# Optimization experiments

Hardware: AMD Instinct MI355X
Metric: run time of the kernel (lower is better)

## Reference

```python
import jax, jax.numpy as jnp
import numpy as np

# Qwen3.5 GatedDeltaNet config (Qwen3-Next linear-attention block)
HIDDEN = 2048
HV, HK = 32, 16          # value heads, key heads (GQA rep = 2)
DK, DV = 128, 128        # key/value head dims
KCONV = 4                # causal depthwise conv kernel
KEY_DIM = HK * DK        # 2048
VAL_DIM = HV * DV        # 4096
CONV_DIM = 2 * KEY_DIM + VAL_DIM  # 8192
EPS = 1e-6


def setup_inputs() -> dict:
    key = jax.random.key(0)
    ks = jax.random.split(key, 9)
    B, S = 2, 1024
    def w(k, shape, sc=0.02):
        return jax.random.normal(k, shape, jnp.float32) * sc
    return {
        "hidden_states": jax.random.normal(ks[0], (B, S, HIDDEN), jnp.float32),
        "conv_w": w(ks[1], (CONV_DIM, 1, KCONV), 0.1),   # depthwise conv1d weight (groups=CONV_DIM, no bias)
        "w_qkv": w(ks[2], (HIDDEN, CONV_DIM)),
        "w_z": w(ks[3], (HIDDEN, VAL_DIM)),
        "w_b": w(ks[4], (HIDDEN, HV)),
        "w_a": w(ks[5], (HIDDEN, HV)),
        "w_out": w(ks[6], (VAL_DIM, HIDDEN)),
        "dt_bias": jnp.ones((HV,), jnp.float32),
        "A_log": jnp.log(jax.random.uniform(ks[7], (HV,), jnp.float32, 1e-3, 16.0)),
        "norm_w": jnp.ones((DV,), jnp.float32),
    }


def _l2norm(x):
    return x / jnp.sqrt(jnp.sum(x * x, axis=-1, keepdims=True) + 1e-6)


def reference(hidden_states, conv_w, w_qkv, w_z, w_b, w_a, w_out, dt_bias, A_log, norm_w):
    B, S, _ = hidden_states.shape
    # input projections
    mixed = hidden_states @ w_qkv                     # [B,S,CONV_DIM]
    z = (hidden_states @ w_z).reshape(B, S, HV, DV)   # gate for RMSNormGated
    b = hidden_states @ w_b                           # [B,S,HV]
    a = hidden_states @ w_a                           # [B,S,HV]

    # causal depthwise conv1d (left pad K-1), then SiLU
    x = mixed.transpose(0, 2, 1)                      # [B,C,S]
    y = jax.lax.conv_general_dilated(
        x, conv_w, window_strides=(1,), padding=[(KCONV - 1, 0)],
        dimension_numbers=("NCH", "OIH", "NCH"), feature_group_count=CONV_DIM)
    mixed = jax.nn.silu(y).transpose(0, 2, 1)         # [B,S,CONV_DIM]

    q, k, v = jnp.split(mixed, [KEY_DIM, 2 * KEY_DIM], axis=-1)
    q = q.reshape(B, S, HK, DK)
    k = k.reshape(B, S, HK, DK)
    v = v.reshape(B, S, HV, DV)

    beta = jax.nn.sigmoid(b)                                    # [B,S,HV]
    g = -jnp.exp(A_log) * jax.nn.softplus(a + dt_bias)          # [B,S,HV], log-decay <= 0

    rep = HV // HK
    q = jnp.repeat(q, rep, axis=2)                              # [B,S,HV,DK]
    k = jnp.repeat(k, rep, axis=2)

    # use_qk_l2norm_in_kernel=True, then standard 1/sqrt(dk) scaling on q
    q = _l2norm(q) * (DK ** -0.5)
    k = _l2norm(k)

    # gated delta-rule recurrence over time (state S: [B,HV,DK,DV])
    qt = q.transpose(1, 0, 2, 3)
    kt = k.transpose(1, 0, 2, 3)
    vt = v.transpose(1, 0, 2, 3)
    gt = g.transpose(1, 0, 2)
    bt = beta.transpose(1, 0, 2)

    S0 = jnp.zeros((B, HV, DK, DV), jnp.float32)

    def step(Sm, inp):
        q_, k_, v_, g_, b_ = inp
        Sm = Sm * jnp.exp(g_)[..., None, None]                  # gated decay
        kv = jnp.einsum('bhk,bhkv->bhv', k_, Sm)                # k^T S (current memory readout)
        delta = (v_ - kv) * b_[..., None]                       # delta-rule update, scaled by beta
        Sm = Sm + jnp.einsum('bhk,bhv->bhkv', k_, delta)        # rank-1 write
        o = jnp.einsum('bhk,bhkv->bhv', q_, Sm)                 # query readout
        return Sm, o

    _, o = jax.lax.scan(step, S0, (qt, kt, vt, gt, bt))
    o = o.transpose(1, 0, 2, 3)                                 # [B,S,HV,DV]

    # RMSNormGated over head_v_dim: gate with silu(z), then RMSNorm
    og = o * jax.nn.silu(z)
    var = jnp.mean(og * og, axis=-1, keepdims=True)
    on = og * jax.lax.rsqrt(var + EPS) * norm_w

    return on.reshape(B, S, VAL_DIM) @ w_out                    # [B,S,HIDDEN]
```

## Files before the change

### kernel.cpp

```cpp
#include <hip/hip_runtime.h>
#include <hip/hip_bf16.h>
#include <cstdint>
#include <type_traits>

#define HIDDEN   2048
#define HV       32
#define HK       16
#define DK       128
#define DV       128
#define KEY_DIM  2048
#define VAL_DIM  4096
#define CONV_DIM 8192
#define NTOK     2048
#define SEQ      1024
#define N1       12288
#define C_CH     64
#define NCHK     (SEQ / C_CH)

typedef __attribute__((ext_vector_type(4))) float f4_t;
typedef __attribute__((ext_vector_type(2))) float f2_t;
typedef __attribute__((ext_vector_type(8))) short bf8_t;
typedef __attribute__((ext_vector_type(16))) float f16acc;
typedef __attribute__((ext_vector_type(4))) unsigned short u16x4;
typedef __attribute__((ext_vector_type(8))) unsigned short u16x8;
typedef __attribute__((ext_vector_type(2))) uint32_t u32x2;
typedef __attribute__((ext_vector_type(4))) uint32_t u32x4;

__device__ __forceinline__ unsigned short f2bf(float f) {
    union { float f; uint32_t u; } a; a.f = f;
    uint32_t u = a.u;
    return (unsigned short)((u + 0x7fff + ((u >> 16) & 1)) >> 16);
}
__device__ __forceinline__ float bf2f(unsigned short h) {
    uint32_t u = ((uint32_t)h) << 16;
    union { uint32_t u; float f; } a; a.u = u;
    return a.f;
}
__device__ __forceinline__ bf8_t lds_frag(const unsigned short* p) {
    u32x2 a = *(const u32x2*)p;
    u32x2 b = *(const u32x2*)(p + 4);
    u32x4 w = {a[0], a[1], b[0], b[1]};
    return __builtin_bit_cast(bf8_t, w);
}

__global__ __launch_bounds__(256) void k_cast_hs(const float* __restrict__ hs,
                                                 unsigned short* __restrict__ out) {
    int i = blockIdx.x * 256 + threadIdx.x;
    f4_t v = ((const f4_t*)hs)[i];
    u16x4 o;
    o[0] = f2bf(v[0]); o[1] = f2bf(v[1]); o[2] = f2bf(v[2]); o[3] = f2bf(v[3]);
    ((u16x4*)out)[i] = o;
}

__global__ __launch_bounds__(256) void k_trans_w1(const float* __restrict__ w_qkv,
                                                  const float* __restrict__ w_z,
                                                  unsigned short* __restrict__ w1t) {
    __shared__ float tile[32][33];
    int tx = threadIdx.x & 31, ty = threadIdx.x >> 5;
    int n0 = blockIdx.x * 32, k0 = blockIdx.y * 32;
    int n = n0 + tx;
#pragma unroll
    for (int i = 0; i < 4; i++) {
        int k = k0 + ty + i * 8;
        float v = (n < CONV_DIM) ? w_qkv[(size_t)k * CONV_DIM + n]
                                 : w_z[(size_t)k * VAL_DIM + (n - CONV_DIM)];
        tile[ty + i * 8][tx] = v;
    }
    __syncthreads();
#pragma unroll
    for (int i = 0; i < 4; i++)
        w1t[(size_t)(n0 + ty + i * 8) * HIDDEN + k0 + tx] = f2bf(tile[tx][ty + i * 8]);
}

__global__ __launch_bounds__(256) void k_trans(const float* __restrict__ src,
                                               unsigned short* __restrict__ dst,
                                               int K, int N) {
    __shared__ float tile[32][33];
    int tx = threadIdx.x & 31, ty = threadIdx.x >> 5;
    int n0 = blockIdx.x * 32, k0 = blockIdx.y * 32;
#pragma unroll
    for (int i = 0; i < 4; i++)
        tile[ty + i * 8][tx] = src[(size_t)(k0 + ty + i * 8) * N + n0 + tx];
    __syncthreads();
#pragma unroll
    for (int i = 0; i < 4; i++)
        dst[(size_t)(n0 + ty + i * 8) * K + k0 + tx] = f2bf(tile[tx][ty + i * 8]);
}

template <typename OT>
__global__ __launch_bounds__(256, 4) void k_gemm_bt(const unsigned short* __restrict__ A,
                                                    const unsigned short* __restrict__ B,
                                                    OT* __restrict__ C, int K, int N) {
    __shared__ unsigned short lA[2][128 * 32];
    __shared__ unsigned short lB[2][128 * 32];
    int tid = threadIdx.x;
    int wave = tid >> 6, lane = tid & 63;
    int nwg = gridDim.x * gridDim.y;
    int lid = blockIdx.y * gridDim.x + blockIdx.x;
    int swz = (lid & 7) * (nwg >> 3) + (lid >> 3);
    int m0 = (swz & 15) * 128, n0 = (swz >> 4) * 128;
    int wm = wave & 1, wn = wave >> 1;
    f4_t acc[4][4];
#pragma unroll
    for (int i = 0; i < 4; i++)
#pragma unroll
        for (int j = 0; j < 4; j++) acc[i][j] = (f4_t){0.f, 0.f, 0.f, 0.f};
    int srow = wave * 16 + (lane >> 2);
    int scol = ((lane & 3) ^ ((lane >> 3) & 3)) * 8;
    int quad = lane >> 4, lrow = lane & 15;
    int rswz = (lrow >> 1) & 3;

    const unsigned short* gA0 = A + (size_t)(m0 + srow) * K + scol;
    const unsigned short* gA1 = A + (size_t)(m0 + 64 + srow) * K + scol;
    const unsigned short* gB0 = B + (size_t)(n0 + srow) * K + scol;
    const unsigned short* gB1 = B + (size_t)(n0 + 64 + srow) * K + scol;

#define GEMM_STAGE(buf, k0)                                                                        \
    do {                                                                                           \
        __builtin_amdgcn_global_load_lds((const __attribute__((address_space(1))) void*)(gA0 + (k0)), \
            (__attribute__((address_space(3))) void*)(&lA[buf][wave * 512]), 16, 0, 0);            \
        __builtin_amdgcn_global_load_lds((const __attribute__((address_space(1))) void*)(gA1 + (k0)), \
            (__attribute__((address_space(3))) void*)(&lA[buf][2048 + wave * 512]), 16, 0, 0);     \
        __builtin_amdgcn_global_load_lds((const __attribute__((address_space(1))) void*)(gB0 + (k0)), \
            (__attribute__((address_space(3))) void*)(&lB[buf][wave * 512]), 16, 0, 0);            \
        __builtin_amdgcn_global_load_lds((const __attribute__((address_space(1))) void*)(gB1 + (k0)), \
            (__attribute__((address_space(3))) void*)(&lB[buf][2048 + wave * 512]), 16, 0, 0);     \
    } while (0)

    GEMM_STAGE(0, 0);
    __syncthreads();

    int cur = 0;
    for (int k0 = 0; k0 < K; k0 += 32) {
        if (k0 + 32 < K) GEMM_STAGE(cur ^ 1, k0 + 32);
        bf8_t af[4], bfv[4];
#pragma unroll
        for (int i = 0; i < 4; i++) {
            int sa = (quad ^ rswz) * 8;
            af[i]  = *(const bf8_t*)&lA[cur][(wm * 64 + i * 16 + lrow) * 32 + sa];
            bfv[i] = *(const bf8_t*)&lB[cur][(wn * 64 + i * 16 + lrow) * 32 + sa];
        }
#pragma unroll
        for (int i = 0; i < 4; i++)
#pragma unroll
            for (int j = 0; j < 4; j++)
                acc[i][j] = __builtin_amdgcn_mfma_f32_16x16x32_bf16(af[i], bfv[j], acc[i][j], 0, 0, 0);
        __syncthreads();
        cur ^= 1;
    }
#undef GEMM_STAGE
#pragma unroll
    for (int i = 0; i < 4; i++) {
        int row_b = m0 + wm * 64 + i * 16 + quad * 4;
#pragma unroll
        for (int j = 0; j < 4; j++) {
            int col = n0 + wn * 64 + j * 16 + lrow;
#pragma unroll
            for (int r = 0; r < 4; r++) {
                if constexpr (std::is_same<OT, float>::value)
                    C[(size_t)(row_b + r) * N + col] = acc[i][j][r];
                else
                    C[(size_t)(row_b + r) * N + col] = f2bf(acc[i][j][r]);
            }
        }
    }
}

#define BG_TOK 4
__global__ __launch_bounds__(256) void k_beta_g(const float* __restrict__ hs,
                                                const float* __restrict__ w_b,
                                                const float* __restrict__ w_a,
                                                const float* __restrict__ dt_bias,
                                                const float* __restrict__ A_log,
                                                float* __restrict__ beta,
                                                float* __restrict__ gval) {
    __shared__ float rows[BG_TOK * HIDDEN];
    __shared__ float part[BG_TOK][64][17];
    int t = threadIdx.x;
    int tok0 = blockIdx.x * BG_TOK;
    {
        const f4_t* src = (const f4_t*)(hs + (size_t)tok0 * HIDDEN);
        f4_t* dst = (f4_t*)rows;
#pragma unroll
        for (int u = 0; u < BG_TOK * HIDDEN / 4 / 256; u++)
            dst[t + u * 256] = src[t + u * 256];
    }
    __syncthreads();
    int hq = t & 15, kp = t >> 4;
    int h0 = hq * 4;
    const float* wsrc = (h0 < 32) ? (w_b + h0) : (w_a + (h0 - 32));
    f4_t acc[BG_TOK];
#pragma unroll
    for (int x = 0; x < BG_TOK; x++) acc[x] = (f4_t){0.f, 0.f, 0.f, 0.f};
    int kbase = kp * 128;
#pragma unroll 4
    for (int i = 0; i < 128; i++) {
        int k = kbase + i;
        f4_t wv = *(const f4_t*)(wsrc + (size_t)k * 32);
#pragma unroll
        for (int x = 0; x < BG_TOK; x++) {
            float r = rows[x * HIDDEN + k];
            acc[x][0] += wv[0] * r;
            acc[x][1] += wv[1] * r;
            acc[x][2] += wv[2] * r;
            acc[x][3] += wv[3] * r;
        }
    }
#pragma unroll
    for (int x = 0; x < BG_TOK; x++)
#pragma unroll
        for (int e = 0; e < 4; e++)
            part[x][h0 + e][kp] = acc[x][e];
    __syncthreads();
    int x = t >> 6, h = t & 63;
    float s = 0.f;
#pragma unroll
    for (int k2 = 0; k2 < 16; k2++) s += part[x][h][k2];
    int tok = tok0 + x;
    if (h < 32) {
        beta[tok * 32 + h] = 1.f / (1.f + expf(-s));
    } else {
        int hh = h - 32;
        float xx = s + dt_bias[hh];
        float sp = (xx > 20.f) ? xx : log1pf(expf(xx));
        gval[tok * 32 + hh] = -expf(A_log[hh]) * sp;
    }
}

#define CCH 32
#define NCHC (SEQ / CCH)
__global__ __launch_bounds__(256) void k_halo(const unsigned short* __restrict__ mixed,
                                              unsigned short* __restrict__ halo) {
    int id = blockIdx.x * 256 + threadIdx.x;
    int c = id & 8191;
    int r = id >> 13;
    int tap = r % 3;
    int ck = (r / 3) % (NCHC - 1);
    int b = r / (3 * (NCHC - 1));
    int s = (ck + 1) * CCH - 1 - tap;
    halo[id] = mixed[(size_t)(b * SEQ + s) * N1 + c];
}

__global__ __launch_bounds__(256) void k_conv(unsigned short* __restrict__ mixed,
                                              const float* __restrict__ cw,
                                              const unsigned short* __restrict__ halo,
                                              float* __restrict__ vbuf) {
    int id = blockIdx.x * 256 + threadIdx.x;
    int c = id & 8191;
    int r = id >> 13;
    int chunk = r & (NCHC - 1), b = r >> 5;
    int s0 = chunk * CCH;
    float w0 = cw[c * 4 + 0], w1 = cw[c * 4 + 1], w2 = cw[c * 4 + 2], w3 = cw[c * 4 + 3];
    float xm1, xm2, xm3;
    if (chunk == 0) {
        xm1 = xm2 = xm3 = 0.f;
    } else {
        const unsigned short* hp = halo + (size_t)(b * (NCHC - 1) + chunk - 1) * 3 * 8192;
        xm1 = bf2f(hp[0 * 8192 + c]); xm2 = bf2f(hp[1 * 8192 + c]); xm3 = bf2f(hp[2 * 8192 + c]);
    }
    unsigned short* col = mixed + (size_t)(b * SEQ + s0) * N1 + c;
    float* vcol = vbuf + (size_t)(b * SEQ + s0) * 4096 + (c - 4096);
#pragma unroll
    for (int s = 0; s < CCH; s++) {
        float x = bf2f(col[(size_t)s * N1]);
        float y = w3 * x + w2 * xm1 + w1 * xm2 + w0 * xm3;
        y = y / (1.f + expf(-y));
        if (c < 4096) col[(size_t)s * N1] = f2bf(y);
        else          vcol[(size_t)s * 4096] = y;
        xm3 = xm2; xm2 = xm1; xm1 = x;
    }
}

__global__ __launch_bounds__(256, 2) void k_prep(const unsigned short* __restrict__ mixed,
                                                 const float* __restrict__ vbuf,
                                                 const float* __restrict__ beta,
                                                 const float* __restrict__ gval,
                                                 unsigned short* __restrict__ Pg,
                                                 unsigned short* __restrict__ KbTg,
                                                 unsigned short* __restrict__ Qbg,
                                                 unsigned short* __restrict__ Wg,
                                                 float* __restrict__ Ug,
                                                 float* __restrict__ Lamg) {
    __shared__ unsigned short lK[64 * 132];
    __shared__ unsigned short lQ[64 * 132];
    __shared__ float lM[64 * 66];
    __shared__ float lG[64], lLam[64], lBeta[64], lKsc[64];

    int blk = blockIdx.x;
    int c = blk & 15, h = (blk >> 4) & 31, b = blk >> 9;
    int hk = h >> 1;
    int t = threadIdx.x;
    int wave = t >> 6, lane = t & 63, half = lane >> 5, lm = lane & 31;
    int s0 = c * C_CH;

    const unsigned short* qptr = mixed + (size_t)(b * SEQ) * N1 + hk * 128;
    const unsigned short* kptr = qptr + 2048;

    {
        int i = t >> 2, c0 = (t & 3) * 32;
        {
            const unsigned short* kr = kptr + (size_t)(s0 + i) * N1 + c0;
            float kv[32];
            float ssk = 0.f;
#pragma unroll
            for (int u = 0; u < 4; u++) {
                u16x8 w = *(const u16x8*)(kr + u * 8);
#pragma unroll
                for (int e = 0; e < 8; e++) { float f = bf2f(w[e]); kv[u * 8 + e] = f; ssk += f * f; }
            }
            ssk += __shfl_xor(ssk, 1); ssk += __shfl_xor(ssk, 2);
            float sck = 1.f / sqrtf(ssk + 1e-6f);
            unsigned short* dK = &lK[i * 132 + c0];
#pragma unroll
            for (int u = 0; u < 8; u++) {
                u16x4 s4;
#pragma unroll
                for (int e = 0; e < 4; e++) s4[e] = f2bf(kv[u * 4 + e] * sck);
                *(u16x4*)(dK + u * 4) = s4;
            }
        }
        {
            const unsigned short* qr = qptr + (size_t)(s0 + i) * N1 + c0;
            float qv[32];
            float ssq = 0.f;
#pragma unroll
            for (int u = 0; u < 4; u++) {
                u16x8 w = *(const u16x8*)(qr + u * 8);
#pragma unroll
                for (int e = 0; e < 8; e++) { float f = bf2f(w[e]); qv[u * 8 + e] = f; ssq += f * f; }
            }
            ssq += __shfl_xor(ssq, 1); ssq += __shfl_xor(ssq, 2);
            float scq = (1.f / sqrtf(ssq + 1e-6f)) * 0.08838834764831845f;
            unsigned short* dQ = &lQ[i * 132 + c0];
#pragma unroll
            for (int u = 0; u < 8; u++) {
                u16x4 s4;
#pragma unroll
                for (int e = 0; e < 4; e++) s4[e] = f2bf(qv[u * 4 + e] * scq);
                *(u16x4*)(dQ + u * 4) = s4;
            }
        }
        if (t < 64) {
            float gv = gval[(size_t)(b * SEQ + s0 + t) * 32 + h];
            float bv = beta[(size_t)(b * SEQ + s0 + t) * 32 + h];
            float x = gv;
#pragma unroll
            for (int d = 1; d < 64; d <<= 1) {
                float y = __shfl_up(x, d);
                if (t >= d) x += y;
            }
            float Gc = __shfl(x, 63);
            lG[t] = x; lLam[t] = expf(x); lBeta[t] = bv; lKsc[t] = expf(Gc - x);
        }
    }
    __syncthreads();

    size_t bhc = (size_t)(b * 32 + h) * 16 + c;
    size_t bkc = (size_t)(b * 16 + hk) * 16 + c;

    for (int job = wave; job < 6; job += 4) {
        int isP = job >= 3 ? 1 : 0;
        int jj = job - (isP ? 3 : 0);
        int ib = (jj == 0) ? 0 : 1;
        int jb = (jj == 2) ? 1 : 0;
        const unsigned short* Ab = isP ? lQ : lK;
        f16acc acc;
#pragma unroll
        for (int r = 0; r < 16; r++) acc[r] = 0.f;
        int arow = ib * 32 + lm, brow = jb * 32 + lm;
#pragma unroll
        for (int k0 = 0; k0 < 128; k0 += 16) {
            bf8_t a = lds_frag(&Ab[arow * 132 + k0 + half * 8]);
            bf8_t bb = lds_frag(&lK[brow * 132 + k0 + half * 8]);
            acc = __builtin_amdgcn_mfma_f32_32x32x16_bf16(a, bb, acc, 0, 0, 0);
        }
        int j = jb * 32 + lm;
        float Gj = lG[j];
#pragma unroll
        for (int r = 0; r < 16; r++) {
            int ml = (r & 3) + 8 * (r >> 2) + 4 * half;
            int i = ib * 32 + ml;
            float f = expf(lG[i] - Gj);
            if (isP) {
                Pg[bhc * 4096 + i * 64 + j] = f2bf((j <= i) ? acc[r] * f : 0.f);
            } else {
                if (j < i) lM[i * 66 + j] = acc[r] * lBeta[i] * f;
            }
        }
    }
#pragma unroll
    for (int u = 0; u < 4; u++) {
        int e = t * 4 + u;
        Pg[bhc * 4096 + (e >> 5) * 64 + 32 + (e & 31)] = 0;
    }

    if ((h & 1) == 0) {
        int i = t >> 2, c0 = (t & 3) * 32;
#pragma unroll
        for (int u = 0; u < 8; u++)
            *(u16x4*)&Qbg[bkc * 8192 + i * 128 + c0 + u * 4] = *(const u16x4*)&lQ[i * 132 + c0 + u * 4];
    }

    {
        int dk = t >> 1, i0 = (t & 1) * 32;
        unsigned short tmp[32];
#pragma unroll
        for (int ii = 0; ii < 32; ii++) {
            int i = i0 + ii;
            tmp[ii] = f2bf(bf2f(lK[i * 132 + dk]) * lKsc[i]);
        }
#pragma unroll
        for (int u = 0; u < 4; u++) {
            u16x8 w;
#pragma unroll
            for (int j = 0; j < 8; j++) w[j] = tmp[u * 8 + j];
            *(u16x8*)&KbTg[bhc * 8192 + dk * 64 + i0 + u * 8] = w;
        }
    }
    if (t < 64) Lamg[bhc * 64 + t] = lLam[t];

    __syncthreads();

    {
        float x[64];
        if (t < 128) {
            const float* vcol = vbuf + (size_t)(b * SEQ + s0) * 4096 + h * 128 + t;
#pragma unroll
            for (int il = 0; il < 64; il++) x[il] = lBeta[il] * vcol[(size_t)il * 4096];
        } else {
            int dk = t - 128;
#pragma unroll
            for (int il = 0; il < 64; il++) x[il] = lBeta[il] * lLam[il] * bf2f(lK[il * 132 + dk]);
        }
#pragma unroll
        for (int il = 1; il < 64; il++)
#pragma unroll
            for (int j = 0; j < il; j++)
                x[il] -= lM[il * 66 + j] * x[j];
        if (t < 128) {
            float* up = Ug + (size_t)(b * SEQ + s0) * 4096 + h * 128 + t;
#pragma unroll
            for (int il = 0; il < 64; il++) up[(size_t)il * 4096] = x[il];
        } else {
            unsigned short* wp = Wg + bhc * 8192 + (t - 128);
#pragma unroll
            for (int il = 0; il < 64; il++) wp[il * 128] = f2bf(-x[il]);
        }
    }
}

__global__ __launch_bounds__(256, 1) void k_state(const unsigned short* __restrict__ Wg,
                                                  const unsigned short* __restrict__ Pg,
                                                  const unsigned short* __restrict__ KbTg,
                                                  const unsigned short* __restrict__ Qbg,
                                                  const float* __restrict__ Lamg,
                                                  float* __restrict__ o) {
    __shared__ unsigned short lSt[32 * 132];
    __shared__ unsigned short lDt[32 * 68];

    int blk = blockIdx.x;
    int vs = blk & 3, h = (blk >> 2) & 31, b = blk >> 7;
    int hk = h >> 1;
    int t = threadIdx.x;
    int wave = t >> 6, lane = t & 63, half = lane >> 5, lm = lane & 31;
    int ib = wave & 1;

    for (int i = t; i < 32 * 132; i += 256) lSt[i] = 0;
    f16acc sacc;
#pragma unroll
    for (int r = 0; r < 16; r++) sacc[r] = 0.f;
    __syncthreads();

    for (int c = 0; c < NCHK; c++) {
        int s0 = c * C_CH;
        size_t bhc = (size_t)(b * 32 + h) * 16 + c;
        size_t bkc = (size_t)(b * 16 + hk) * 16 + c;

        const unsigned short* Ag = (wave < 2) ? (Wg + bhc * 8192) : (Qbg + bkc * 8192);
        bf8_t afr[8];
#pragma unroll
        for (int kk = 0; kk < 8; kk++)
            afr[kk] = *(const bf8_t*)&Ag[(ib * 32 + lm) * 128 + kk * 16 + half * 8];
        bf8_t ktfr[4];
#pragma unroll
        for (int u = 0; u < 4; u++)
            ktfr[u] = *(const bf8_t*)&KbTg[bhc * 8192 + (wave * 32 + lm) * 64 + u * 16 + half * 8];
        bf8_t pfr[4];
        f4_t lamv[4];
        if (wave >= 2) {
#pragma unroll
            for (int u = 0; u < 4; u++)
                pfr[u] = *(const bf8_t*)&Pg[bhc * 4096 + (ib * 32 + lm) * 64 + u * 16 + half * 8];
#pragma unroll
            for (int q = 0; q < 4; q++)
                lamv[q] = *(const f4_t*)&Lamg[bhc * 64 + ib * 32 + q * 8 + half * 4];
        }
        float lamC = Lamg[bhc * 64 + 63];

        f16acc wacc;
        if (wave < 2) {
            const float* up = o + (size_t)(b * SEQ + s0 + ib * 32) * 4096 + h * 128 + vs * 32 + lm;
#pragma unroll
            for (int r = 0; r < 16; r++) {
                int ml = (r & 3) + 8 * (r >> 2) + 4 * half;
                wacc[r] = up[(size_t)ml * 4096];
            }
        } else {
#pragma unroll
            for (int r = 0; r < 16; r++) wacc[r] = 0.f;
        }
#pragma unroll
        for (int kk = 0; kk < 8; kk++) {
            bf8_t bb = lds_frag(&lSt[lm * 132 + kk * 16 + half * 8]);
            wacc = __builtin_amdgcn_mfma_f32_32x32x16_bf16(afr[kk], bb, wacc, 0, 0, 0);
        }
        if (wave < 2) {
#pragma unroll
            for (int r = 0; r < 16; r++) {
                int ml = (r & 3) + 8 * (r >> 2) + 4 * half;
                lDt[lm * 68 + ib * 32 + ml] = f2bf(wacc[r]);
            }
        }
        __syncthreads();

        if (wave >= 2) {
#pragma unroll
            for (int r = 0; r < 16; r++) wacc[r] *= lamv[r >> 2][r & 3];
#pragma unroll
            for (int u = 0; u < 4; u++) {
                bf8_t bb = lds_frag(&lDt[lm * 68 + u * 16 + half * 8]);
                wacc = __builtin_amdgcn_mfma_f32_32x32x16_bf16(pfr[u], bb, wacc, 0, 0, 0);
            }
#pragma unroll
            for (int r = 0; r < 16; r++) {
                int ml = (r & 3) + 8 * (r >> 2) + 4 * half;
                o[(size_t)(b * SEQ + s0 + ib * 32 + ml) * 4096 + h * 128 + vs * 32 + lm] = wacc[r];
            }
        }
#pragma unroll
        for (int r = 0; r < 16; r++) sacc[r] *= lamC;
#pragma unroll
        for (int u = 0; u < 4; u++) {
            bf8_t bb = lds_frag(&lDt[lm * 68 + u * 16 + half * 8]);
            sacc = __builtin_amdgcn_mfma_f32_32x32x16_bf16(ktfr[u], bb, sacc, 0, 0, 0);
        }
#pragma unroll
        for (int r = 0; r < 16; r++) {
            int ml = (r & 3) + 8 * (r >> 2) + 4 * half;
            lSt[lm * 132 + 32 * wave + ml] = f2bf(sacc[r]);
        }
        __syncthreads();
    }
}

__global__ __launch_bounds__(256) void k_gnorm(const float* __restrict__ o,
                                               const unsigned short* __restrict__ mixed,
                                               const float* __restrict__ norm_w,
                                               unsigned short* __restrict__ on) {
    int tok = blockIdx.x, t = threadIdx.x;
    int hh = t >> 3, ln = t & 7;
    const f4_t* op = (const f4_t*)(o + (size_t)tok * 4096 + hh * 128 + ln * 16);
    const unsigned short* zp = mixed + (size_t)tok * N1 + 8192 + hh * 128 + ln * 16;
    u16x8 zr0 = *(const u16x8*)zp;
    u16x8 zr1 = *(const u16x8*)(zp + 8);
    float og[16];
    float ss = 0.f;
#pragma unroll
    for (int i = 0; i < 4; i++) {
        f4_t ov = op[i];
#pragma unroll
        for (int j = 0; j < 4; j++) {
            int e = i * 4 + j;
            float z = (e < 8) ? bf2f(zr0[e]) : bf2f(zr1[e - 8]);
            float g = ov[j] * (z / (1.f + expf(-z)));
            og[e] = g;
            ss += g * g;
        }
    }
    ss += __shfl_xor(ss, 1); ss += __shfl_xor(ss, 2); ss += __shfl_xor(ss, 4);
    float r = 1.f / sqrtf(ss * (1.f / 128.f) + 1e-6f);
    unsigned short* onp = on + (size_t)tok * 4096 + hh * 128 + ln * 16;
    u16x8 a, bb;
#pragma unroll
    for (int j = 0; j < 8; j++) a[j] = f2bf(og[j] * r * norm_w[ln * 16 + j]);
#pragma unroll
    for (int j = 0; j < 8; j++) bb[j] = f2bf(og[8 + j] * r * norm_w[ln * 16 + 8 + j]);
    ((u16x8*)onp)[0] = a;
    ((u16x8*)onp)[1] = bb;
}

extern "C" void kernel_launch(void* const* d_in, const int* in_sizes, int n_in,
                              void* d_out, int out_size, void* d_ws, size_t ws_size,
                              hipStream_t stream) {
    const float* hs      = (const float*)d_in[0];
    const float* conv_w  = (const float*)d_in[1];
    const float* w_qkv   = (const float*)d_in[2];
    const float* w_z     = (const float*)d_in[3];
    const float* w_b     = (const float*)d_in[4];
    const float* w_a     = (const float*)d_in[5];
    const float* w_out   = (const float*)d_in[6];
    const float* dt_bias = (const float*)d_in[7];
    const float* A_log   = (const float*)d_in[8];
    const float* norm_w  = (const float*)d_in[9];
    float* out = (float*)d_out;

    char* ws = (char*)d_ws;
    unsigned short* hs_bf = (unsigned short*)ws; ws += (size_t)NTOK * HIDDEN * 2;
    unsigned short* w1t   = (unsigned short*)ws; ws += (size_t)N1 * HIDDEN * 2;
    unsigned short* wot   = (unsigned short*)ws; ws += (size_t)HIDDEN * VAL_DIM * 2;
    unsigned short* mixed = (unsigned short*)ws; ws += (size_t)NTOK * N1 * 2;
    float* vbuf           = (float*)ws;          ws += (size_t)NTOK * 4096 * 4;
    float* beta           = (float*)ws;          ws += (size_t)NTOK * 32 * 4;
    float* gval           = (float*)ws;          ws += (size_t)NTOK * 32 * 4;
    unsigned short* halo  = (unsigned short*)ws; ws += (size_t)2 * (NCHC - 1) * 3 * 8192 * 2;
    float* o_buf          = (float*)ws;          ws += (size_t)NTOK * VAL_DIM * 4;
    unsigned short* on_bf = (unsigned short*)ws; ws += (size_t)NTOK * VAL_DIM * 2;

    char* al = (char*)hs_bf;
    unsigned short* Wg    = (unsigned short*)al; al += (size_t)1024 * 8192 * 2;
    unsigned short* Pg    = (unsigned short*)al; al += (size_t)1024 * 4096 * 2;
    unsigned short* KbTg  = (unsigned short*)al; al += (size_t)1024 * 8192 * 2;
    unsigned short* Qbg   = (unsigned short*)al; al += (size_t)512 * 8192 * 2;
    float* Lamg           = (float*)halo;

    k_cast_hs<<<dim3(NTOK * HIDDEN / 4 / 256), 256, 0, stream>>>(hs, hs_bf);
    k_trans_w1<<<dim3(N1 / 32, HIDDEN / 32), 256, 0, stream>>>(w_qkv, w_z, w1t);
    k_trans<<<dim3(HIDDEN / 32, VAL_DIM / 32), 256, 0, stream>>>(w_out, wot, VAL_DIM, HIDDEN);
    k_gemm_bt<unsigned short><<<dim3(NTOK / 128, N1 / 128), 256, 0, stream>>>(hs_bf, w1t, mixed, HIDDEN, N1);
    k_beta_g<<<dim3(NTOK / BG_TOK), 256, 0, stream>>>(hs, w_b, w_a, dt_bias, A_log, beta, gval);
    k_halo<<<dim3(2 * (NCHC - 1) * 3 * 8192 / 256), 256, 0, stream>>>(mixed, halo);
    k_conv<<<dim3(2 * NCHC * 8192 / 256), 256, 0, stream>>>(mixed, conv_w, halo, vbuf);
    k_prep<<<dim3(1024), 256, 0, stream>>>(mixed, vbuf, beta, gval, Pg, KbTg, Qbg, Wg, o_buf, Lamg);
    k_state<<<dim3(256), 256, 0, stream>>>(Wg, Pg, KbTg, Qbg, Lamg, o_buf);
    k_gnorm<<<dim3(NTOK), 256, 0, stream>>>(o_buf, mixed, norm_w, on_bf);
    k_gemm_bt<float><<<dim3(NTOK / 128, HIDDEN / 128), 256, 0, stream>>>(on_bf, wot, out, VAL_DIM, HIDDEN);
}
```

Before: 552.9 us.

## Triple-buffer GEMM LDS stages with explicit vmcnt waits for deeper prefetch

Changes the bf16 GEMM main loop from double to triple buffering, issuing global-to-LDS loads two K-steps ahead. The full __syncthreads is replaced with targeted s_waitcnt vmcnt counts plus raw barriers, so a wave only waits for the stage it is about to consume. The goal is to hide more global memory latency behind MFMA work. In exchange, LDS per block rises by half and the occupancy hint drops from 4 to 3 blocks. Correctness also depends on the hand-counted vmcnt values and on the compiler not reordering memory ops across the raw barriers.

Measured after the change: 559.7 us. About the same (+1.2%).

```diff
diff --git a/kernel.cpp b/kernel.cpp
--- a/kernel.cpp
+++ b/kernel.cpp
@@ -88,11 +88,11 @@
 }
 
 template <typename OT>
-__global__ __launch_bounds__(256, 4) void k_gemm_bt(const unsigned short* __restrict__ A,
+__global__ __launch_bounds__(256, 3) void k_gemm_bt(const unsigned short* __restrict__ A,
                                                     const unsigned short* __restrict__ B,
                                                     OT* __restrict__ C, int K, int N) {
-    __shared__ unsigned short lA[2][128 * 32];
-    __shared__ unsigned short lB[2][128 * 32];
+    __shared__ unsigned short lA[3][128 * 32];
+    __shared__ unsigned short lB[3][128 * 32];
     int tid = threadIdx.x;
     int wave = tid >> 6, lane = tid & 63;
     int nwg = gridDim.x * gridDim.y;
@@ -127,26 +127,37 @@
             (__attribute__((address_space(3))) void*)(&lB[buf][2048 + wave * 512]), 16, 0, 0);     \
     } while (0)
 
+    int iters = K >> 5;
     GEMM_STAGE(0, 0);
-    __syncthreads();
+    if (iters > 1) GEMM_STAGE(1, 32);
 
     int cur = 0;
-    for (int k0 = 0; k0 < K; k0 += 32) {
-        if (k0 + 32 < K) GEMM_STAGE(cur ^ 1, k0 + 32);
+    for (int i = 0; i < iters; ++i) {
+        int k0 = i << 5;
+        if (i + 2 < iters) {
+            int nxt = cur + 2; if (nxt >= 3) nxt -= 3;
+            GEMM_STAGE(nxt, k0 + 64);
+            asm volatile("s_waitcnt vmcnt(8)" ::: "memory");
+        } else if (i + 1 < iters) {
+            asm volatile("s_waitcnt vmcnt(4)" ::: "memory");
+        } else {
+            asm volatile("s_waitcnt vmcnt(0)" ::: "memory");
+        }
+        __builtin_amdgcn_s_barrier();
         bf8_t af[4], bfv[4];
 #pragma unroll
-        for (int i = 0; i < 4; i++) {
+        for (int ii = 0; ii < 4; ii++) {
             int sa = (quad ^ rswz) * 8;
-            af[i]  = *(const bf8_t*)&lA[cur][(wm * 64 + i * 16 + lrow) * 32 + sa];
-            bfv[i] = *(const bf8_t*)&lB[cur][(wn * 64 + i * 16 + lrow) * 32 + sa];
-        }
-#pragma unroll
-        for (int i = 0; i < 4; i++)
+            af[ii]  = *(const bf8_t*)&lA[cur][(wm * 64 + ii * 16 + lrow) * 32 + sa];
+            bfv[ii] = *(const bf8_t*)&lB[cur][(wn * 64 + ii * 16 + lrow) * 32 + sa];
+        }
+#pragma unroll
+        for (int ii = 0; ii < 4; ii++)
 #pragma unroll
             for (int j = 0; j < 4; j++)
-                acc[i][j] = __builtin_amdgcn_mfma_f32_16x16x32_bf16(af[i], bfv[j], acc[i][j], 0, 0, 0);
-        __syncthreads();
-        cur ^= 1;
+                acc[ii][j] = __builtin_amdgcn_mfma_f32_16x16x32_bf16(af[ii], bfv[j], acc[ii][j], 0, 0, 0);
+        __builtin_amdgcn_s_barrier();
+        cur = cur + 1; if (cur >= 3) cur = 0;
     }
 #undef GEMM_STAGE
 #pragma unroll
```
